# Kernel tuning notes

Measured on AMD Instinct MI355X. Metric: run time of the kernel, lower is better.

The kernel has to match this reference:

```python
import jax, jax.numpy as jnp
import numpy as np

NUM_HEADS = 8
H_DIM = 24
COORDS_DIM = 3
NUM_W_PER_DIST = 8
BLOCK_SIZE = 128
N_HASHES = 3
N = 32768
HASH_DIM = H_DIM + (COORDS_DIM - 1) + 2  # q/k augmented with RPE coordinate terms


def layernorm(x, g, b, eps=1e-5):
    mu = x.mean(-1, keepdims=True)
    var = ((x - mu) ** 2).mean(-1, keepdims=True)
    return (x - mu) * jax.lax.rsqrt(var + eps) * g + b


def setup_inputs() -> dict:
    key = jax.random.key(0)
    ks = jax.random.split(key, 16)
    d, H = H_DIM, NUM_HEADS
    s = lambda i, shape, scale: jax.random.normal(ks[i], shape, jnp.float32) * scale
    return {
        "x": s(0, (N, d), 1.0),
        "coords": jax.random.uniform(ks[1], (N, COORDS_DIM), jnp.float32),
        "norm1_g": jnp.ones((d,), jnp.float32),
        "norm1_b": jnp.zeros((d,), jnp.float32),
        "Wq": s(2, (d, H * d), d ** -0.5),
        "Wk": s(3, (d, H * d), d ** -0.5),
        "Wv": s(4, (d, H * d), d ** -0.5),
        "w_rpe_W": s(5, (H * d, (COORDS_DIM - 1) * NUM_W_PER_DIST), 0.3),
        "Wo": s(6, (H * d, d), (H * d) ** -0.5),
        "bo": jnp.zeros((d,), jnp.float32),
        "norm2_g": jnp.ones((d,), jnp.float32),
        "norm2_b": jnp.zeros((d,), jnp.float32),
        "ff_W1": s(7, (d, d), d ** -0.5),
        "ff_b1": jnp.zeros((d,), jnp.float32),
        "ff_W2": s(8, (d, d), d ** -0.5),
        "ff_b2": jnp.zeros((d,), jnp.float32),
        "alphas": s(9, (N_HASHES, H, HASH_DIM), 1.0),  # E2LSH projection vectors
    }


def hept_attention(q, k, v, coords, w_rpe_W, alphas):
    # q,k,v: [n, H*d]. HEPT: fold RPE exp(-w*||dp||^2) into augmented q/k, then
    # n_hashes rounds of LSH sort + block-local attention, combined by softmax
    # over each round's log-normalizer (Reformer-style).
    n = q.shape[0]
    H, d, B = NUM_HEADS, H_DIM, BLOCK_SIZE
    nb = n // B
    q = q.reshape(n, H, d).transpose(1, 0, 2) * (d ** -0.5)  # [H,n,d]
    k = k.reshape(n, H, d).transpose(1, 0, 2)
    v = v.reshape(n, H, d).transpose(1, 0, 2)
    # per-head non-negative distance weights from w_rpe (mixture collapsed)
    Wm = w_rpe_W.reshape(H, d, COORDS_DIM - 1, NUM_W_PER_DIST)
    w = jnp.mean(Wm, axis=(1, 3)) ** 2                        # [H, c-1]
    p = coords[:, 1:]                                          # [n, c-1]
    sqn = jnp.einsum("hc,nc,nc->hn", w, p, p)                # w*||p||^2
    qp = jnp.sqrt(2.0) * jnp.sqrt(w)[:, None, :] * p[None]     # [H,n,c-1]
    ones = jnp.ones((H, n, 1), q.dtype)
    # q_hat.k_hat = q.k + 2*w*p_i.p_j - w|p_i|^2 - w|p_j|^2 = q.k - w*||p_i-p_j||^2
    q_hat = jnp.concatenate([q, qp, -sqn[..., None], ones], -1)  # [H,n,HASH_DIM]
    k_hat = jnp.concatenate([k, qp, ones, -sqn[..., None]], -1)
    outs, zs = [], []
    for r in range(N_HASHES):
        a = alphas[r]                                          # [H, HASH_DIM]
        iq = jnp.argsort(jnp.einsum("hne,he->hn", q_hat, a), -1)
        ik = jnp.argsort(jnp.einsum("hne,he->hn", k_hat, a), -1)
        qs = jnp.take_along_axis(q_hat, iq[..., None], 1).reshape(H, nb, B, -1)
        ks = jnp.take_along_axis(k_hat, ik[..., None], 1).reshape(H, nb, B, -1)
        vs = jnp.take_along_axis(v, ik[..., None], 1).reshape(H, nb, B, d)
        logits = jnp.einsum("hbqe,hbke->hbqk", qs, ks)         # [H,nb,B,B]
        z = jax.nn.logsumexp(logits, -1).reshape(H, n)
        o = jnp.einsum("hbqk,hbkd->hbqd", jax.nn.softmax(logits, -1), vs).reshape(H, n, d)
        inv = jnp.argsort(iq, -1)                              # unsort to input order
        outs.append(jnp.take_along_axis(o, inv[..., None], 1))
        zs.append(jnp.take_along_axis(z, inv, 1))
    wts = jax.nn.softmax(jnp.stack(zs), axis=0)[..., None]     # [R,H,n,1]
    out = (jnp.stack(outs) * wts).sum(0)                       # [H,n,d]
    return out.transpose(1, 0, 2).reshape(n, H * d)


def reference(x, coords, norm1_g, norm1_b, Wq, Wk, Wv, w_rpe_W, Wo, bo,
              norm2_g, norm2_b, ff_W1, ff_b1, ff_W2, ff_b2, alphas):
    xn = layernorm(x, norm1_g, norm1_b)
    q, k, v = xn @ Wq, xn @ Wk, xn @ Wv
    aggr = hept_attention(q, k, v, coords, w_rpe_W, alphas) @ Wo + bo
    x = x + aggr  # dropout is identity in eval mode
    h = layernorm(x, norm2_g, norm2_b)
    ff = jax.nn.relu(h @ ff_W1 + ff_b1) @ ff_W2 + ff_b2
    return x + ff
```

## Files before the change

kernel.cpp:

```cpp
#include <hip/hip_runtime.h>
#include <math.h>

#define NPT 32768
#define NH 8
#define HD 24
#define EDIM 28
#define NHASH 3
#define NSEG 48
#define NRH 24

typedef unsigned long long u64;
typedef unsigned short ushort;
typedef __attribute__((__vector_size__(8 * sizeof(short)))) short bf16x8;
typedef __attribute__((__vector_size__(4 * sizeof(float)))) float floatx4;

__device__ __forceinline__ ushort f2bf(float f) {
    unsigned u = __float_as_uint(f);
    unsigned r = u + 0x7FFF + ((u >> 16) & 1);
    return (ushort)(r >> 16);
}
__device__ __forceinline__ float us2f(ushort u) {
    return __uint_as_float(((unsigned)u) << 16);
}

__global__ __launch_bounds__(256) void k0b(
    const float* __restrict__ wrpe, const float* __restrict__ Wq,
    const float* __restrict__ Wk, const float* __restrict__ alphas,
    double* __restrict__ w64, double* __restrict__ cqp64,
    double* __restrict__ Aq, double* __restrict__ Ak, double* __restrict__ ct) {
    __shared__ double sw[16], sc[16];
    int t = threadIdx.x;
    if (t < 16) {
        int h = t >> 1, c = t & 1;
        double s = 0.0;
        for (int i = 0; i < 24; i++)
            for (int j = 0; j < 8; j++)
                s += (double)wrpe[(h * 24 + i) * 16 + c * 8 + j];
        double m = s / 192.0;
        sw[t] = m * m;
        sc[t] = sqrt(2.0) * fabs(m);
        w64[t] = sw[t];
        cqp64[t] = sc[t];
    }
    __syncthreads();
    const double QSCALE = 1.0 / sqrt(24.0);
    for (int idx = t; idx < 24 * NRH; idx += 256) {
        int i = idx / NRH, rh = idx % NRH;
        int h = rh & 7;
        double aq = 0.0, ak = 0.0;
        for (int e = 0; e < 24; e++) {
            double al = (double)alphas[rh * 28 + e];
            aq += (double)Wq[i * 192 + h * 24 + e] * al;
            ak += (double)Wk[i * 192 + h * 24 + e] * al;
        }
        Aq[idx] = aq * QSCALE;
        Ak[idx] = ak;
    }
    if (t < NRH) {
        int h = t & 7;
        ct[t * 4 + 0] = (double)alphas[t * 28 + 24] * sc[h * 2 + 0];
        ct[t * 4 + 1] = (double)alphas[t * 28 + 25] * sc[h * 2 + 1];
        ct[t * 4 + 2] = (double)alphas[t * 28 + 26];
        ct[t * 4 + 3] = (double)alphas[t * 28 + 27];
    }
}

__global__ __launch_bounds__(256) void k1b(
    const float* __restrict__ x, const float* __restrict__ g,
    const float* __restrict__ b, float* __restrict__ xnf) {
    __shared__ float sGB[48];
    int t = threadIdx.x;
    if (t < 24) { sGB[t] = g[t]; sGB[24 + t] = b[t]; }
    __syncthreads();
    int wv = t >> 6, l = t & 63;
    int half = l >> 5, e = l & 31;
    for (int it = 0; it < 8; it++) {
        int n = blockIdx.x * 64 + it * 8 + wv * 2 + half;
        float xv = (e < 24) ? x[(u64)n * 24 + e] : 0.f;
        float s = xv;
        s += __shfl_xor(s, 1); s += __shfl_xor(s, 2); s += __shfl_xor(s, 4);
        s += __shfl_xor(s, 8); s += __shfl_xor(s, 16);
        float mu = s * (1.0f / 24.0f);
        float d = (e < 24) ? (xv - mu) : 0.f;
        float v = d * d;
        v += __shfl_xor(v, 1); v += __shfl_xor(v, 2); v += __shfl_xor(v, 4);
        v += __shfl_xor(v, 8); v += __shfl_xor(v, 16);
        float rstd = 1.0f / sqrtf(v * (1.0f / 24.0f) + 1e-5f);
        if (e < 24) xnf[(u64)n * 24 + e] = d * rstd * sGB[e] + sGB[24 + e];
    }
}

__global__ __launch_bounds__(512) void k2s(
    const float* __restrict__ x, const float* __restrict__ n1g,
    const float* __restrict__ n1b, const float* __restrict__ coords,
    const double* __restrict__ Aq, const double* __restrict__ Ak,
    const double* __restrict__ ct, const double* __restrict__ w64,
    u64* __restrict__ keys) {
    __shared__ double sA[2][24][NRH];
    __shared__ double sCt[NRH][4];
    __shared__ double sW64[16];
    __shared__ double sGB[48];
    __shared__ double sXn[8][24];
    int t = threadIdx.x;
    for (int i = t; i < 24 * NRH; i += 512) sA[0][i / NRH][i % NRH] = Aq[i];
    for (int i = t; i < 24 * NRH; i += 512) sA[1][i / NRH][i % NRH] = Ak[i];
    for (int i = t; i < NRH * 4; i += 512) sCt[i / 4][i % 4] = ct[i];
    if (t < 16) sW64[t] = w64[t];
    if (t < 24) { sGB[t] = (double)n1g[t]; sGB[24 + t] = (double)n1b[t]; }
    __syncthreads();
    int wv = t >> 6, l = t & 63;
    for (int g = 0; g < 8; g++) {
        int n = blockIdx.x * 64 + g * 8 + wv;
        double xv = (l < 24) ? (double)x[(u64)n * 24 + l] : 0.0;
        double s = xv;
        s += __shfl_xor(s, 1); s += __shfl_xor(s, 2); s += __shfl_xor(s, 4);
        s += __shfl_xor(s, 8); s += __shfl_xor(s, 16);
        double mu = s / 24.0;
        double d = (l < 24) ? (xv - mu) : 0.0;
        double v2 = d * d;
        v2 += __shfl_xor(v2, 1); v2 += __shfl_xor(v2, 2); v2 += __shfl_xor(v2, 4);
        v2 += __shfl_xor(v2, 8); v2 += __shfl_xor(v2, 16);
        double rstd = 1.0 / sqrt(v2 / 24.0 + 1e-5);
        if (l < 24) sXn[wv][l] = d * rstd * sGB[l] + sGB[24 + l];
        double p0 = (double)coords[(u64)n * 3 + 1];
        double p1 = (double)coords[(u64)n * 3 + 2];
        if (l < 2 * NRH) {
            int qk = l / NRH, rh = l % NRH;
            int h = rh & 7;
            double sqn = sW64[2 * h] * p0 * p0 + sW64[2 * h + 1] * p1 * p1;
            double acc = sCt[rh][0] * p0 + sCt[rh][1] * p1;
            acc += qk ? (sCt[rh][2] - sqn * sCt[rh][3]) : (sCt[rh][3] - sqn * sCt[rh][2]);
            for (int i = 0; i < 24; i++) acc += sXn[wv][i] * sA[qk][i][rh];
            u64 u = (u64)__double_as_longlong(acc);
            if (u >> 63) u = ~u; else u |= 0x8000000000000000ULL;
            u64 key = (u & ~(u64)32767) | (u64)n;
            keys[(u64)l * NPT + n] = key;
        }
    }
}

#define K2P_PTS 64
__global__ __launch_bounds__(640) void k2p(
    const float* __restrict__ xnf,
    const float* __restrict__ Wq, const float* __restrict__ Wk,
    const float* __restrict__ Wv, const float* __restrict__ coords,
    const double* __restrict__ w64, const double* __restrict__ cqp64,
    ushort* __restrict__ qhatB, ushort* __restrict__ khatB, ushort* __restrict__ varrB) {
    int t = threadIdx.x;
    int n0 = blockIdx.x * K2P_PTS;
    if (t < 576) {
        int m = t / 192, jj = t % 192;
        const float* W = (m == 0) ? Wq : ((m == 1) ? Wk : Wv);
        float wc[24];
#pragma unroll
        for (int i = 0; i < 24; i++) wc[i] = W[i * 192 + jj];
        const float scale = (m == 0) ? (float)(1.0 / sqrt(24.0)) : 1.0f;
        int h = jj / 24, e = jj % 24;
        ushort* outp = (m == 0) ? qhatB : ((m == 1) ? khatB : varrB);
        const int ostride = (m == 2) ? 24 : 32;
        ushort* obase = outp + (u64)h * NPT * ostride + e;
        for (int p = 0; p < K2P_PTS; p++) {
            int n = n0 + p;
            const float* xr = xnf + (u64)n * 24;
            float acc = 0.f;
#pragma unroll
            for (int i = 0; i < 24; i++) acc += xr[i] * wc[i];
            obase[(u64)n * ostride] = f2bf(acc * scale);
        }
    } else {
        int l = t - 576;
        int h2 = l >> 3, e2 = 24 + (l & 7);
        double c0 = cqp64[h2 * 2], c1 = cqp64[h2 * 2 + 1];
        double wa = w64[h2 * 2], wb = w64[h2 * 2 + 1];
        ushort* qb = qhatB + (u64)h2 * NPT * 32 + e2;
        ushort* kb = khatB + (u64)h2 * NPT * 32 + e2;
        for (int p = 0; p < K2P_PTS; p++) {
            int n = n0 + p;
            double p0 = (double)coords[(u64)n * 3 + 1];
            double p1 = (double)coords[(u64)n * 3 + 2];
            float qv, kv;
            if (e2 < 26) {
                int c = e2 - 24;
                float qp = (float)((c ? c1 : c0) * (c ? p1 : p0));
                qv = qp; kv = qp;
            } else if (e2 < 28) {
                double sqn = wa * p0 * p0 + wb * p1 * p1;
                if (e2 == 26) { qv = (float)(-sqn); kv = 1.0f; }
                else          { qv = 1.0f; kv = (float)(-sqn); }
            } else {
                qv = 0.0f; kv = 0.0f;
            }
            qb[(u64)n * 32] = f2bf(qv);
            kb[(u64)n * 32] = f2bf(kv);
        }
    }
}

__device__ __forceinline__ u64 shflx64(u64 v, int d) {
    int lo = __shfl_xor((int)(unsigned)v, d);
    int hi = __shfl_xor((int)(unsigned)(v >> 32), d);
    return ((u64)(unsigned)hi << 32) | (unsigned)lo;
}
__device__ __forceinline__ void cswap(u64& a, u64& b, bool up) {
    if ((a > b) == up) { u64 tmp = a; a = b; b = tmp; }
}
__device__ __forceinline__ u64* sslot(u64* s, int i) {
    int a = i << 3;
    a ^= ((a >> 9) & 7) << 4;
    return (u64*)((char*)s + a);
}
__device__ __forceinline__ void reg_passes(u64 e[8], int ib, int K, int jmax) {
    for (int j = jmax; j >= 1; j >>= 1) {
#pragma unroll
        for (int k = 0; k < 8; k++)
            if ((k & j) == 0) cswap(e[k], e[k | j], ((ib + k) & K) == 0);
    }
}
__device__ __forceinline__ void shfl_passes(u64 e[8], int t, int segoff, int K, int jhi, int jlo) {
    for (int j = jhi; j >= jlo; j >>= 1) {
        int d = j >> 3;
        bool lower = (t & d) == 0;
        bool up = ((segoff + ((t & ~d) << 3)) & K) == 0;
        bool keepmin = (lower == up);
#pragma unroll
        for (int k = 0; k < 8; k++) {
            u64 o = shflx64(e[k], d);
            bool ownsm = e[k] < o;
            e[k] = (ownsm == keepmin) ? e[k] : o;
        }
    }
}

__global__ __launch_bounds__(1024) void sort_local_full(u64* keys) {
    __shared__ u64 s[8192];
    int t = threadIdx.x;
    u64 gbase = (u64)blockIdx.x * 8192;
    int segoff = (int)(gbase & 32767);
    int ib = segoff + t * 8;
    u64 e[8];
#pragma unroll
    for (int k = 0; k < 8; k++) e[k] = keys[gbase + t * 8 + k];
    reg_passes(e, ib, 2, 1);
    reg_passes(e, ib, 4, 2);
    reg_passes(e, ib, 8, 4);
    for (int K = 16; K <= 512; K <<= 1) {
        shfl_passes(e, t, segoff, K, K >> 1, 8);
        reg_passes(e, ib, K, 4);
    }
#pragma unroll
    for (int k = 0; k < 8; k++) *sslot(s, t * 8 + k) = e[k];
    __syncthreads();
    for (int K = 1024; K <= 8192; K <<= 1) {
        for (int j = K >> 1; j >= 512; j >>= 1) {
            for (int p = t; p < 4096; p += 1024) {
                int i = ((p & ~(j - 1)) << 1) | (p & (j - 1));
                int i2 = i | j;
                bool up = (((segoff + i) & K) == 0);
                u64 a = *sslot(s, i), b = *sslot(s, i2);
                if ((a > b) == up) { *sslot(s, i) = b; *sslot(s, i2) = a; }
            }
            __syncthreads();
        }
#pragma unroll
        for (int k = 0; k < 8; k++) e[k] = *sslot(s, t * 8 + k);
        shfl_passes(e, t, segoff, K, 256, 8);
        reg_passes(e, ib, K, 4);
        if (K < 8192) {
#pragma unroll
            for (int k = 0; k < 8; k++) *sslot(s, t * 8 + k) = e[k];
            __syncthreads();
        } else {
#pragma unroll
            for (int k = 0; k < 8; k++) keys[gbase + t * 8 + k] = e[k];
        }
    }
}

__global__ __launch_bounds__(1024) void sort_local_tail(u64* keys, int K, int minj) {
    __shared__ u64 s[8192];
    int t = threadIdx.x;
    u64 gbase = (u64)blockIdx.x * 8192;
    int segoff = (int)(gbase & 32767);
    int ib = segoff + t * 8;
    for (int i = t; i < 8192; i += 1024) *sslot(s, i) = keys[gbase + i];
    __syncthreads();
    for (int j = 4096; j >= 512; j >>= 1) {
        for (int p = t; p < 4096; p += 1024) {
            int i = ((p & ~(j - 1)) << 1) | (p & (j - 1));
            int i2 = i | j;
            bool up = (((segoff + i) & K) == 0);
            u64 a = *sslot(s, i), b = *sslot(s, i2);
            if ((a > b) == up) { *sslot(s, i) = b; *sslot(s, i2) = a; }
        }
        __syncthreads();
    }
    u64 e[8];
#pragma unroll
    for (int k = 0; k < 8; k++) e[k] = *sslot(s, t * 8 + k);
    shfl_passes(e, t, segoff, K, 256, minj >= 8 ? minj : 8);
    if (minj < 8) reg_passes(e, ib, K, 4);
#pragma unroll
    for (int k = 0; k < 8; k++) keys[gbase + t * 8 + k] = e[k];
}

__global__ void sort_global_pass(u64* keys, int k, int j) {
    int p = blockIdx.x * blockDim.x + threadIdx.x;
    if (p >= NSEG * NPT / 2) return;
    int i = ((p & ~(j - 1)) << 1) | (p & (j - 1));
    int l2 = i | j;
    bool up = (((i & 32767) & k) == 0);
    u64 a = keys[i], b = keys[l2];
    if ((a > b) == up) { keys[i] = b; keys[l2] = a; }
}

__global__ void sort_global2(u64* keys) {
    int p = blockIdx.x * blockDim.x + threadIdx.x;
    if (p >= NSEG * 8192) return;
    int seg = p >> 13, c = p & 8191;
    u64 base = (u64)seg * 32768 + c;
    u64 e0 = keys[base];
    u64 e1 = keys[base + 8192];
    u64 e2 = keys[base + 16384];
    u64 e3 = keys[base + 24576];
    u64 tmp;
    if (e0 > e2) { tmp = e0; e0 = e2; e2 = tmp; }
    if (e1 > e3) { tmp = e1; e1 = e3; e3 = tmp; }
    if (e0 > e1) { tmp = e0; e0 = e1; e1 = tmp; }
    if (e2 > e3) { tmp = e2; e2 = e3; e3 = tmp; }
    keys[base] = e0;
    keys[base + 8192] = e1;
    keys[base + 16384] = e2;
    keys[base + 24576] = e3;
}

#define VT_STRIDE 136
#define P_STRIDE 72
__global__ __launch_bounds__(256, 3) void k3_attn(
    const u64* __restrict__ keys, const ushort* __restrict__ qhatB,
    const ushort* __restrict__ khatB, const ushort* __restrict__ varrB,
    ushort* __restrict__ ozB) {
    int rh3 = blockIdx.x % 24;
    int b = blockIdx.x / 24;
    int h = rh3 & 7, r = rh3 >> 3;
    __shared__ __align__(16) char smem[6528 + 18432 + 1024];
    short* sVt = (short*)smem;
    short* sP  = (short*)(smem + 6528);
    int* qidx  = (int*)(smem + 6528 + 18432);
    int* kidx  = qidx + 128;
    int t = threadIdx.x;
    int segQ = r * 8 + h, segK = 24 + r * 8 + h;
    if (t < 128) {
        qidx[t] = (int)(keys[(u64)segQ * NPT + b * 128 + t] & 32767ULL);
    } else {
        int i = t - 128;
        kidx[i] = (int)(keys[(u64)segK * NPT + b * 128 + i] & 32767ULL);
    }
    __syncthreads();

    int wave = t >> 6, L = t & 63;
    int quad = L >> 4, n16 = L & 15;

    const bf16x8* Qg = (const bf16x8*)(qhatB + (u64)h * NPT * 32);
    const bf16x8* Kg = (const bf16x8*)(khatB + (u64)h * NPT * 32);
    bf16x8 afr[2];
#pragma unroll
    for (int rtg = 0; rtg < 2; rtg++) {
        int qi = qidx[wave * 32 + rtg * 16 + n16];
        afr[rtg] = Qg[(u64)qi * 4 + quad];
    }
    bf16x8 bfr[8];
#pragma unroll
    for (int ct = 0; ct < 8; ct++) {
        int ki = kidx[ct * 16 + n16];
        bfr[ct] = Kg[(u64)ki * 4 + quad];
    }
    {
        int row = t & 127, half = t >> 7;
        int ki = kidx[row];
        const ushort* vr = varrB + ((u64)h * NPT + ki) * 24 + half * 12;
        ushort vv[12];
#pragma unroll
        for (int e = 0; e < 12; e++) vv[e] = vr[e];
#pragma unroll
        for (int e = 0; e < 12; e++) sVt[(half * 12 + e) * VT_STRIDE + row] = (short)vv[e];
    }
    __syncthreads();

    floatx4 acc[2][8];
#pragma unroll
    for (int rtg = 0; rtg < 2; rtg++)
#pragma unroll
        for (int ct = 0; ct < 8; ct++)
            acc[rtg][ct] = (floatx4){0.f, 0.f, 0.f, 0.f};
#pragma unroll
    for (int ct = 0; ct < 8; ct++) {
#pragma unroll
        for (int rtg = 0; rtg < 2; rtg++)
            acc[rtg][ct] = __builtin_amdgcn_mfma_f32_16x16x32_bf16(afr[rtg], bfr[ct], acc[rtg][ct], 0, 0, 0);
    }

    float mrow[2][4], srow[2][4];
#pragma unroll
    for (int rtg = 0; rtg < 2; rtg++) {
#pragma unroll
        for (int rg = 0; rg < 4; rg++) {
            float m = -1e30f;
#pragma unroll
            for (int ct = 0; ct < 8; ct++) m = fmaxf(m, acc[rtg][ct][rg]);
            m = fmaxf(m, __shfl_xor(m, 1));
            m = fmaxf(m, __shfl_xor(m, 2));
            m = fmaxf(m, __shfl_xor(m, 4));
            m = fmaxf(m, __shfl_xor(m, 8));
            mrow[rtg][rg] = m;
            float s = 0.0f;
            int row = wave * 32 + rtg * 16 + quad * 4 + rg;
#pragma unroll
            for (int ct = 0; ct < 8; ct++) {
                float p = __expf(acc[rtg][ct][rg] - m);
                s += p;
                if (ct < 4) sP[row * P_STRIDE + ct * 16 + n16] = (short)f2bf(p);
            }
            s += __shfl_xor(s, 1);
            s += __shfl_xor(s, 2);
            s += __shfl_xor(s, 4);
            s += __shfl_xor(s, 8);
            srow[rtg][rg] = s;
        }
    }

    floatx4 occ[2][2];
#pragma unroll
    for (int rtg = 0; rtg < 2; rtg++)
#pragma unroll
        for (int ct2 = 0; ct2 < 2; ct2++)
            occ[rtg][ct2] = (floatx4){0.f, 0.f, 0.f, 0.f};
#pragma unroll
    for (int ks = 0; ks < 2; ks++) {
        bf16x8 bv[2], av[2];
#pragma unroll
        for (int ct2 = 0; ct2 < 2; ct2++)
            bv[ct2] = *(const bf16x8*)(sVt + (ct2 * 16 + n16) * VT_STRIDE + ks * 32 + quad * 8);
#pragma unroll
        for (int rtg = 0; rtg < 2; rtg++)
            av[rtg] = *(const bf16x8*)(sP + (wave * 32 + rtg * 16 + n16) * P_STRIDE + ks * 32 + quad * 8);
#pragma unroll
        for (int rtg = 0; rtg < 2; rtg++)
#pragma unroll
            for (int ct2 = 0; ct2 < 2; ct2++)
                occ[rtg][ct2] = __builtin_amdgcn_mfma_f32_16x16x32_bf16(av[rtg], bv[ct2], occ[rtg][ct2], 0, 0, 0);
    }
#pragma unroll
    for (int rtg = 0; rtg < 2; rtg++) {
#pragma unroll
        for (int rg = 0; rg < 4; rg++) {
            int row = wave * 32 + rtg * 16 + quad * 4 + rg;
#pragma unroll
            for (int ct = 4; ct < 8; ct++) {
                float p = __expf(acc[rtg][ct][rg] - mrow[rtg][rg]);
                sP[row * P_STRIDE + (ct - 4) * 16 + n16] = (short)f2bf(p);
            }
        }
    }
#pragma unroll
    for (int ks = 2; ks < 4; ks++) {
        bf16x8 bv[2], av[2];
#pragma unroll
        for (int ct2 = 0; ct2 < 2; ct2++)
            bv[ct2] = *(const bf16x8*)(sVt + (ct2 * 16 + n16) * VT_STRIDE + ks * 32 + quad * 8);
#pragma unroll
        for (int rtg = 0; rtg < 2; rtg++)
            av[rtg] = *(const bf16x8*)(sP + (wave * 32 + rtg * 16 + n16) * P_STRIDE + (ks - 2) * 32 + quad * 8);
#pragma unroll
        for (int rtg = 0; rtg < 2; rtg++)
#pragma unroll
            for (int ct2 = 0; ct2 < 2; ct2++)
                occ[rtg][ct2] = __builtin_amdgcn_mfma_f32_16x16x32_bf16(av[rtg], bv[ct2], occ[rtg][ct2], 0, 0, 0);
    }

#pragma unroll
    for (int rtg = 0; rtg < 2; rtg++) {
#pragma unroll
        for (int rg = 0; rg < 4; rg++) {
            int row = wave * 32 + rtg * 16 + quad * 4 + rg;
            int oi = qidx[row];
            float inv = 1.0f / srow[rtg][rg];
            ushort* orow = ozB + ((u64)segQ * NPT + oi) * 32;
#pragma unroll
            for (int ct2 = 0; ct2 < 2; ct2++) {
                int col = ct2 * 16 + n16;
                if (col < 24) orow[col] = f2bf(occ[rtg][ct2][rg] * inv);
            }
            if (n16 == 0)
                *(float*)(orow + 24) = mrow[rtg][rg] + __logf(srow[rtg][rg]);
        }
    }
}

#define K4PTS 32
__global__ __launch_bounds__(256) void k4_final(
    const ushort* __restrict__ ozB,
    const float* __restrict__ x,
    const float* __restrict__ Wo, const float* __restrict__ bo,
    const float* __restrict__ g2, const float* __restrict__ b2,
    const float* __restrict__ W1, const float* __restrict__ b1f,
    const float* __restrict__ W2, const float* __restrict__ b2f,
    float* __restrict__ out) {
    __shared__ float sWo[192 * 24];
    __shared__ float sW1[24 * 24], sW2[24 * 24];
    __shared__ float sB[5 * 24];
    __shared__ float attn[K4PTS][193];
    __shared__ float xrow[K4PTS][25];
    __shared__ float h2row[K4PTS][25];
    __shared__ float ffrow[K4PTS][25];
    int t = threadIdx.x;
    int base = blockIdx.x * K4PTS;
    for (int i = t; i < 4608; i += 256) sWo[i] = Wo[i];
    for (int i = t; i < 576; i += 256) { sW1[i] = W1[i]; sW2[i] = W2[i]; }
    if (t < 24) {
        sB[t] = bo[t]; sB[24 + t] = g2[t]; sB[48 + t] = b2[t];
        sB[72 + t] = b1f[t]; sB[96 + t] = b2f[t];
    }
    {
        int p = t >> 3, h = t & 7;
        int n = base + p;
        const ushort* r0 = ozB + ((u64)(0 * 8 + h) * NPT + n) * 32;
        const ushort* r1 = ozB + ((u64)(1 * 8 + h) * NPT + n) * 32;
        const ushort* r2 = ozB + ((u64)(2 * 8 + h) * NPT + n) * 32;
        float z0 = *(const float*)(r0 + 24);
        float z1 = *(const float*)(r1 + 24);
        float z2 = *(const float*)(r2 + 24);
        float zm = fmaxf(z0, fmaxf(z1, z2));
        float e0 = __expf(z0 - zm), e1 = __expf(z1 - zm), e2 = __expf(z2 - zm);
        float inv = 1.0f / (e0 + e1 + e2);
        float w0 = e0 * inv, w1 = e1 * inv, w2 = e2 * inv;
#pragma unroll
        for (int e = 0; e < 24; e++)
            attn[p][h * 24 + e] = w0 * us2f(r0[e]) + w1 * us2f(r1[e]) + w2 * us2f(r2[e]);
    }
    __syncthreads();
    int p = t >> 3, oe = t & 7;
    int n = base + p;
    {
        float a0 = 0.f, a1 = 0.f, a2 = 0.f;
        for (int i = 0; i < 192; i++) {
            float ai = attn[p][i];
            a0 += ai * sWo[i * 24 + oe];
            a1 += ai * sWo[i * 24 + oe + 8];
            a2 += ai * sWo[i * 24 + oe + 16];
        }
        xrow[p][oe]      = x[n * 24 + oe]      + a0 + sB[oe];
        xrow[p][oe + 8]  = x[n * 24 + oe + 8]  + a1 + sB[oe + 8];
        xrow[p][oe + 16] = x[n * 24 + oe + 16] + a2 + sB[oe + 16];
    }
    float mu, rstd;
    {
        float s = xrow[p][oe] + xrow[p][oe + 8] + xrow[p][oe + 16];
        s += __shfl_xor(s, 1); s += __shfl_xor(s, 2); s += __shfl_xor(s, 4);
        mu = s / 24.0f;
        float v0 = xrow[p][oe] - mu, v1 = xrow[p][oe + 8] - mu, v2 = xrow[p][oe + 16] - mu;
        float v = v0 * v0 + v1 * v1 + v2 * v2;
        v += __shfl_xor(v, 1); v += __shfl_xor(v, 2); v += __shfl_xor(v, 4);
        rstd = 1.0f / sqrtf(v / 24.0f + 1e-5f);
    }
    h2row[p][oe]      = (xrow[p][oe] - mu)      * rstd * sB[24 + oe]      + sB[48 + oe];
    h2row[p][oe + 8]  = (xrow[p][oe + 8] - mu)  * rstd * sB[24 + oe + 8]  + sB[48 + oe + 8];
    h2row[p][oe + 16] = (xrow[p][oe + 16] - mu) * rstd * sB[24 + oe + 16] + sB[48 + oe + 16];
    {
        float a0 = sB[72 + oe], a1 = sB[72 + oe + 8], a2 = sB[72 + oe + 16];
        for (int i = 0; i < 24; i++) {
            float hi = h2row[p][i];
            a0 += hi * sW1[i * 24 + oe];
            a1 += hi * sW1[i * 24 + oe + 8];
            a2 += hi * sW1[i * 24 + oe + 16];
        }
        ffrow[p][oe]      = fmaxf(a0, 0.f);
        ffrow[p][oe + 8]  = fmaxf(a1, 0.f);
        ffrow[p][oe + 16] = fmaxf(a2, 0.f);
    }
    {
        float a0 = sB[96 + oe], a1 = sB[96 + oe + 8], a2 = sB[96 + oe + 16];
        for (int i = 0; i < 24; i++) {
            float fi = ffrow[p][i];
            a0 += fi * sW2[i * 24 + oe];
            a1 += fi * sW2[i * 24 + oe + 8];
            a2 += fi * sW2[i * 24 + oe + 16];
        }
        out[n * 24 + oe]      = xrow[p][oe]      + a0;
        out[n * 24 + oe + 8]  = xrow[p][oe + 8]  + a1;
        out[n * 24 + oe + 16] = xrow[p][oe + 16] + a2;
    }
}

extern "C" void kernel_launch(void* const* d_in, const int* in_sizes, int n_in,
                              void* d_out, int out_size, void* d_ws, size_t ws_size,
                              hipStream_t stream) {
    const float* x      = (const float*)d_in[0];
    const float* coords = (const float*)d_in[1];
    const float* n1g    = (const float*)d_in[2];
    const float* n1b    = (const float*)d_in[3];
    const float* Wq     = (const float*)d_in[4];
    const float* Wk     = (const float*)d_in[5];
    const float* Wv     = (const float*)d_in[6];
    const float* wrpe   = (const float*)d_in[7];
    const float* Wo     = (const float*)d_in[8];
    const float* bo     = (const float*)d_in[9];
    const float* n2g    = (const float*)d_in[10];
    const float* n2b    = (const float*)d_in[11];
    const float* W1     = (const float*)d_in[12];
    const float* b1     = (const float*)d_in[13];
    const float* W2     = (const float*)d_in[14];
    const float* b2     = (const float*)d_in[15];
    const float* alphas = (const float*)d_in[16];

    char* ws = (char*)d_ws;
    size_t off = 0;
    auto alloc = [&](size_t bytes) -> void* {
        void* p = ws + off;
        off = (off + bytes + 255) & ~(size_t)255;
        return p;
    };
    double* w64   = (double*)alloc(256);
    double* cqp   = (double*)alloc(256);
    double* Aq    = (double*)alloc(24 * NRH * 8);
    double* Ak    = (double*)alloc(24 * NRH * 8);
    double* ct    = (double*)alloc(NRH * 4 * 8);
    float*  xnf   = (float*)alloc((size_t)NPT * 24 * 4);
    ushort* qhatB = (ushort*)alloc((size_t)NH * NPT * 32 * 2);
    ushort* khatB = (ushort*)alloc((size_t)NH * NPT * 32 * 2);
    ushort* varrB = (ushort*)alloc((size_t)NH * NPT * 24 * 2);
    u64*    keys  = (u64*)alloc((size_t)NSEG * NPT * 8);
    ushort* ozB   = (ushort*)alloc((size_t)NHASH * NH * NPT * 32 * 2);
    if (off > ws_size) return;

    k0b<<<1, 256, 0, stream>>>(wrpe, Wq, Wk, alphas, w64, cqp, Aq, Ak, ct);
    k1b<<<NPT / 64, 256, 0, stream>>>(x, n1g, n1b, xnf);
    k2s<<<NPT / 64, 512, 0, stream>>>(x, n1g, n1b, coords, Aq, Ak, ct, w64, keys);
    k2p<<<NPT / K2P_PTS, 640, 0, stream>>>(xnf, Wq, Wk, Wv, coords, w64, cqp,
                                           qhatB, khatB, varrB);
    sort_local_full<<<192, 1024, 0, stream>>>(keys);
    sort_global_pass<<<3072, 256, 0, stream>>>(keys, 16384, 8192);
    sort_local_tail<<<192, 1024, 0, stream>>>(keys, 16384, 1);
    sort_global2<<<NSEG * 8192 / 256, 256, 0, stream>>>(keys);
    sort_local_tail<<<192, 1024, 0, stream>>>(keys, 32768, 128);
    k3_attn<<<256 * 8 * 3, 256, 0, stream>>>(keys, qhatB, khatB, varrB, ozB);
    k4_final<<<NPT / K4PTS, 256, 0, stream>>>(ozB, x, Wo, bo, n2g, n2b,
                                              W1, b1, W2, b2, (float*)d_out);
}
```

Before: 327.3 us.

## Pad V rows to 32 for vector loads, vectorize k4 Wo matvec, raise k3 occupancy

V is now stored with a 32-element row stride so k3_attn can gather each key's V row with three 16-byte vector loads from 128 threads, replacing 12 scalar 2-byte loads per thread. k4_final transposes Wo in shared memory and pads the rows so the 192-long dot products use float4 shared-memory reads. k3_attn's launch bound asks for 6 blocks per SM instead of 3, which may force register spilling. The padded V buffer uses more workspace and lanes 24-31 of each row are never written.

Result: slower. 357.8 us (+9.3%).

```diff
diff --git a/kernel.cpp b/kernel.cpp
--- a/kernel.cpp
+++ b/kernel.cpp
@@ -157,15 +157,14 @@
         const float scale = (m == 0) ? (float)(1.0 / sqrt(24.0)) : 1.0f;
         int h = jj / 24, e = jj % 24;
         ushort* outp = (m == 0) ? qhatB : ((m == 1) ? khatB : varrB);
-        const int ostride = (m == 2) ? 24 : 32;
-        ushort* obase = outp + (u64)h * NPT * ostride + e;
+        ushort* obase = outp + (u64)h * NPT * 32 + e;
         for (int p = 0; p < K2P_PTS; p++) {
             int n = n0 + p;
             const float* xr = xnf + (u64)n * 24;
             float acc = 0.f;
 #pragma unroll
             for (int i = 0; i < 24; i++) acc += xr[i] * wc[i];
-            obase[(u64)n * ostride] = f2bf(acc * scale);
+            obase[(u64)n * 32] = f2bf(acc * scale);
         }
     } else {
         int l = t - 576;
@@ -335,7 +334,7 @@
 
 #define VT_STRIDE 136
 #define P_STRIDE 72
-__global__ __launch_bounds__(256, 3) void k3_attn(
+__global__ __launch_bounds__(256, 6) void k3_attn(
     const u64* __restrict__ keys, const ushort* __restrict__ qhatB,
     const ushort* __restrict__ khatB, const ushort* __restrict__ varrB,
     ushort* __restrict__ ozB) {
@@ -374,15 +373,16 @@
         int ki = kidx[ct * 16 + n16];
         bfr[ct] = Kg[(u64)ki * 4 + quad];
     }
-    {
-        int row = t & 127, half = t >> 7;
-        int ki = kidx[row];
-        const ushort* vr = varrB + ((u64)h * NPT + ki) * 24 + half * 12;
-        ushort vv[12];
-#pragma unroll
-        for (int e = 0; e < 12; e++) vv[e] = vr[e];
-#pragma unroll
-        for (int e = 0; e < 12; e++) sVt[(half * 12 + e) * VT_STRIDE + row] = (short)vv[e];
+    if (t < 128) {
+        int ki = kidx[t];
+        const bf16x8* vr = (const bf16x8*)(varrB + ((u64)h * NPT + ki) * 32);
+        bf16x8 v0 = vr[0], v1 = vr[1], v2 = vr[2];
+#pragma unroll
+        for (int e = 0; e < 8; e++) {
+            sVt[e * VT_STRIDE + t]        = v0[e];
+            sVt[(8 + e) * VT_STRIDE + t]  = v1[e];
+            sVt[(16 + e) * VT_STRIDE + t] = v2[e];
+        }
     }
     __syncthreads();
 
@@ -497,6 +497,7 @@
 }
 
 #define K4PTS 32
+#define AT_STR 196
 __global__ __launch_bounds__(256) void k4_final(
     const ushort* __restrict__ ozB,
     const float* __restrict__ x,
@@ -505,16 +506,16 @@
     const float* __restrict__ W1, const float* __restrict__ b1f,
     const float* __restrict__ W2, const float* __restrict__ b2f,
     float* __restrict__ out) {
-    __shared__ float sWo[192 * 24];
+    __shared__ __align__(16) float sWoT[24][AT_STR];
     __shared__ float sW1[24 * 24], sW2[24 * 24];
     __shared__ float sB[5 * 24];
-    __shared__ float attn[K4PTS][193];
+    __shared__ __align__(16) float attn[K4PTS][AT_STR];
     __shared__ float xrow[K4PTS][25];
     __shared__ float h2row[K4PTS][25];
     __shared__ float ffrow[K4PTS][25];
     int t = threadIdx.x;
     int base = blockIdx.x * K4PTS;
-    for (int i = t; i < 4608; i += 256) sWo[i] = Wo[i];
+    for (int i = t; i < 4608; i += 256) sWoT[i % 24][i / 24] = Wo[i];
     for (int i = t; i < 576; i += 256) { sW1[i] = W1[i]; sW2[i] = W2[i]; }
     if (t < 24) {
         sB[t] = bo[t]; sB[24 + t] = g2[t]; sB[48 + t] = b2[t];
@@ -541,13 +542,20 @@
     int p = t >> 3, oe = t & 7;
     int n = base + p;
     {
-        float a0 = 0.f, a1 = 0.f, a2 = 0.f;
-        for (int i = 0; i < 192; i++) {
-            float ai = attn[p][i];
-            a0 += ai * sWo[i * 24 + oe];
-            a1 += ai * sWo[i * 24 + oe + 8];
-            a2 += ai * sWo[i * 24 + oe + 16];
-        }
+        const floatx4* ap = (const floatx4*)&attn[p][0];
+        const floatx4* w0p = (const floatx4*)&sWoT[oe][0];
+        const floatx4* w1p = (const floatx4*)&sWoT[oe + 8][0];
+        const floatx4* w2p = (const floatx4*)&sWoT[oe + 16][0];
+        floatx4 A0 = {0.f, 0.f, 0.f, 0.f}, A1 = A0, A2 = A0;
+        for (int ii = 0; ii < 48; ii++) {
+            floatx4 av = ap[ii];
+            A0 += av * w0p[ii];
+            A1 += av * w1p[ii];
+            A2 += av * w2p[ii];
+        }
+        float a0 = A0[0] + A0[1] + A0[2] + A0[3];
+        float a1 = A1[0] + A1[1] + A1[2] + A1[3];
+        float a2 = A2[0] + A2[1] + A2[2] + A2[3];
         xrow[p][oe]      = x[n * 24 + oe]      + a0 + sB[oe];
         xrow[p][oe + 8]  = x[n * 24 + oe + 8]  + a1 + sB[oe + 8];
         xrow[p][oe + 16] = x[n * 24 + oe + 16] + a2 + sB[oe + 16];
@@ -627,7 +635,7 @@
     float*  xnf   = (float*)alloc((size_t)NPT * 24 * 4);
     ushort* qhatB = (ushort*)alloc((size_t)NH * NPT * 32 * 2);
     ushort* khatB = (ushort*)alloc((size_t)NH * NPT * 32 * 2);
-    ushort* varrB = (ushort*)alloc((size_t)NH * NPT * 24 * 2);
+    ushort* varrB = (ushort*)alloc((size_t)NH * NPT * 32 * 2);
     u64*    keys  = (u64*)alloc((size_t)NSEG * NPT * 8);
     ushort* ozB   = (ushort*)alloc((size_t)NHASH * NH * NPT * 32 * 2);
     if (off > ws_size) return;
```
